# Kernel optimization log

Measured on AMD Instinct MI355X. Metric: run time of the kernel, lower is better.

The kernel has to match this reference:

```python
import jax, jax.numpy as jnp
import numpy as np

B, H, N, D, RPE = 2, 8, 4096, 64, 64
LAYERS = 3


def _rms(x):
    # SimpleRMSNorm: x / sqrt(mean(x^2) + eps), no learned scale
    return x / jnp.sqrt(jnp.mean(x * x, axis=-1, keepdims=True) + 1e-8)


def setup_inputs() -> dict:
    key = jax.random.key(0)
    ks = jax.random.split(key, 7)
    s = 1.0 / np.sqrt(RPE)
    return {
        "x": jax.random.normal(ks[0], (B, H, N, D), dtype=jnp.float32),
        "w_in": jax.random.normal(ks[1], (1, RPE), dtype=jnp.float32) * 0.5,
        "b_in": jax.random.normal(ks[2], (RPE,), dtype=jnp.float32) * 0.02,
        "w_hid": jax.random.normal(ks[3], (LAYERS, RPE, RPE), dtype=jnp.float32) * s,
        "b_hid": jax.random.normal(ks[4], (LAYERS, RPE), dtype=jnp.float32) * 0.02,
        "w_out": jax.random.normal(ks[5], (RPE, H * D), dtype=jnp.float32) * s,
        "b_out": jax.random.normal(ks[6], (H * D,), dtype=jnp.float32) * 0.02,
    }


def reference(x, w_in, b_in, w_hid, b_hid, w_out, b_out):
    n = x.shape[-2]
    dt = x.dtype

    def rpe(idx):  # idx: (m, 1) relative-position features
        h = idx @ w_in + b_in  # (m, RPE)
        for i in range(LAYERS):  # non-residual: x = layer(x)
            h = jax.nn.relu(_rms(h)) @ w_hid[i] + b_hid[i]
        h = jax.nn.relu(_rms(h)) @ w_out + b_out  # (m, H*D)
        return h.reshape(-1, H, D).transpose(1, 0, 2)  # (H, m, D)

    zero_idx = jnp.ones((1, 1), dt)
    pos_idx = (1.0 / jnp.arange(2, n + 1, dtype=dt)).reshape(n - 1, 1)
    neg_idx = (-1.0 / jnp.arange(n, 1, -1, dtype=dt)).reshape(n - 1, 1)

    zero_k = rpe(zero_idx)  # (H, 1, D); used for both T[0] slots like the torch code
    a = jnp.concatenate([zero_k, rpe(pos_idx), zero_k, rpe(neg_idx)], axis=1)  # (H, 2n, D)
    # act_type='none' -> identity activation on a

    # Toeplitz matvec as circular conv of length 2n via FFT
    y = jnp.fft.rfft(x, 2 * n, axis=-2)          # (B, H, n+1, D) complex
    v = jnp.fft.rfft(a, 2 * n, axis=-2)[None]    # (1, H, n+1, D) complex
    out = jnp.fft.irfft(v * y, 2 * n, axis=-2)[:, :, :n, :]
    return out.astype(dt)
```

## Files before the change

### kernel.cpp

```cpp
#include <hip/hip_runtime.h>

#define N_SEQ 4096
#define N_FFT 8192
#define LAYERS 3
#define FT 512

#define IDX2(i) ((i) + (((i) >> 5) << 1))

#define WSYNC() { asm volatile("s_waitcnt lgkmcnt(0)" ::: "memory"); __builtin_amdgcn_wave_barrier(); }

__device__ __forceinline__ float2 cmulf(float2 a, float2 b) {
    return make_float2(fmaf(a.x, b.x, -a.y * b.y), fmaf(a.x, b.y, a.y * b.x));
}
__device__ __forceinline__ float2 cmulcf(float2 a, float2 b) {
    return make_float2(fmaf(a.x, b.x, a.y * b.y), fmaf(a.y, b.x, -a.x * b.y));
}
__device__ __forceinline__ float2 f2a(float2 a, float2 b) { return make_float2(a.x + b.x, a.y + b.y); }
__device__ __forceinline__ float2 f2s(float2 a, float2 b) { return make_float2(a.x - b.x, a.y - b.y); }

__device__ __forceinline__ void twchain(int np, float2* T)
{
    float c1, s1;
    __sincosf(-7.6699039394282061e-4f * (float)np, &s1, &c1);
    T[1] = make_float2(c1, s1);
    T[2] = cmulf(T[1], T[1]);
    T[3] = cmulf(T[2], T[1]);
    T[4] = cmulf(T[2], T[2]);
    T[5] = cmulf(T[3], T[2]);
    T[6] = cmulf(T[3], T[3]);
    T[7] = cmulf(T[4], T[3]);
}

__device__ __forceinline__ void ahead8(const float* x, int np, float2* X)
{
    const float R2 = 0.70710678118654752f;
    float p0 = x[0] + x[4], q0 = x[0] - x[4];
    float p1 = x[2] + x[6], q1 = x[2] - x[6];
    float r0 = x[1] + x[5], t0 = x[1] - x[5];
    float r1 = x[3] + x[7], t1 = x[3] - x[7];
    float e0 = p0 + p1, e2 = p0 - p1;
    float o0 = r0 + r1, o2 = r0 - r1;
    float rm = R2 * (t0 - t1), rp = R2 * (t0 + t1);
    X[0] = make_float2(e0 + o0, 0.f);
    X[4] = make_float2(e0 - o0, 0.f);
    X[2] = make_float2(e2, -o2);
    X[6] = make_float2(e2,  o2);
    X[1] = make_float2(q0 + rm, -q1 - rp);
    X[5] = make_float2(q0 - rm, -q1 + rp);
    X[3] = make_float2(q0 - rm,  q1 - rp);
    X[7] = make_float2(q0 + rm,  q1 + rp);
    float2 T[8];
    twchain(np, T);
#pragma unroll
    for (int q = 1; q < 8; ++q) X[q] = cmulf(X[q], T[q]);
}

__device__ __forceinline__ void zhead8(const float2* z, int np, float2* X)
{
    const float R2 = 0.70710678118654752f;
    float2 A0 = f2a(z[0], z[2]);
    float2 A2 = f2s(z[0], z[2]);
    float2 A1 = make_float2(z[0].x + z[2].y, z[0].y - z[2].x);
    float2 A3 = make_float2(z[0].x - z[2].y, z[0].y + z[2].x);
    float2 B0 = f2a(z[1], z[3]);
    float2 bm = f2s(z[1], z[3]);
    float2 B2 = make_float2(bm.y, -bm.x);
    float2 u1 = make_float2(z[1].x + z[3].y, z[1].y - z[3].x);
    float2 B1 = make_float2(R2 * (u1.x + u1.y), R2 * (u1.y - u1.x));
    float2 u3 = make_float2(z[1].x - z[3].y, z[1].y + z[3].x);
    float2 B3 = make_float2(R2 * (u3.y - u3.x), -R2 * (u3.x + u3.y));
    X[0] = f2a(A0, B0); X[4] = f2s(A0, B0);
    X[1] = f2a(A1, B1); X[5] = f2s(A1, B1);
    X[2] = f2a(A2, B2); X[6] = f2s(A2, B2);
    X[3] = f2a(A3, B3); X[7] = f2s(A3, B3);
    float2 T[8];
    twchain(np, T);
#pragma unroll
    for (int q = 1; q < 8; ++q) X[q] = cmulf(X[q], T[q]);
}

__device__ __forceinline__ void ihead8(const float2* v, int np, float2* u)
{
    const float R2 = 0.70710678118654752f;
    float2 T[8];
    twchain(np, T);
    float2 V[8];
    V[0] = v[0];
#pragma unroll
    for (int q = 1; q < 8; ++q) V[q] = cmulcf(v[q], T[q]);
    float2 s0 = f2a(V[0], V[4]), d0 = f2s(V[0], V[4]);
    float2 s1 = f2a(V[1], V[5]), d1 = f2s(V[1], V[5]);
    float2 s2 = f2a(V[2], V[6]), d2 = f2s(V[2], V[6]);
    float2 s3 = f2a(V[3], V[7]), d3 = f2s(V[3], V[7]);
    u[0] = f2a(f2a(s0, s1), f2a(s2, s3));
    u[2] = make_float2((s0.x - s2.x) - (s1.y - s3.y),
                       (s0.y - s2.y) + (s1.x - s3.x));
    float m1 = R2 * (d1.x - d1.y), p1 = R2 * (d1.x + d1.y);
    float m3 = R2 * (d3.x - d3.y), p3 = R2 * (d3.x + d3.y);
    u[1] = make_float2(d0.x + m1 - d2.y - p3, d0.y + p1 + d2.x + m3);
    u[3] = make_float2(d0.x - p1 + d2.y + m3, d0.y + m1 - d2.x + p3);
}

__device__ __forceinline__ void tail4_fwd(float2* y)
{
#pragma unroll
    for (int g = 0; g < 16; g += 4) {
        float2 a = f2a(y[g],     y[g + 2]);
        float2 b = f2s(y[g],     y[g + 2]);
        float2 c = f2a(y[g + 1], y[g + 3]);
        float2 w = f2s(y[g + 1], y[g + 3]);
        float2 d = make_float2(w.y, -w.x);
        y[g]     = f2a(a, c);
        y[g + 1] = f2a(b, d);
        y[g + 2] = f2s(a, c);
        y[g + 3] = f2s(b, d);
    }
}
__device__ __forceinline__ void tail4_inv(float2* y)
{
#pragma unroll
    for (int g = 0; g < 16; g += 4) {
        float2 a = f2a(y[g],     y[g + 2]);
        float2 b = f2s(y[g],     y[g + 2]);
        float2 c = f2a(y[g + 1], y[g + 3]);
        float2 d = f2s(y[g + 1], y[g + 3]);
        float2 id = make_float2(-d.y, d.x);
        y[g]     = f2a(a, c);
        y[g + 2] = f2s(a, c);
        y[g + 1] = f2a(b, id);
        y[g + 3] = f2s(b, id);
    }
}

template<int M>
__device__ __forceinline__ void wpass16_fwd(float2* buf, int C, int lane)
{
    const int Q = M >> 4;
    const int j = lane & (Q - 1);
    const int base = C + (lane / Q) * M + j;
    const float KR[4] = {1.f, 0.9238795325f, 0.7071067812f, 0.3826834324f};
    const float KI[4] = {0.f, -0.3826834324f, -0.7071067812f, -0.9238795325f};
    float xr[4][4], xi[4][4];
#pragma unroll
    for (int a = 0; a < 4; ++a)
#pragma unroll
        for (int b = 0; b < 4; ++b) {
            float2 v = buf[IDX2(base + a * (M >> 2) + b * Q)];
            xr[a][b] = v.x; xi[a][b] = v.y;
        }
    float cj, sj;
    __sincosf(-6.283185307179586f / (float)M * (float)j, &sj, &cj);
#pragma unroll
    for (int b = 0; b < 4; ++b) {
        float c1 = cj * KR[b] - sj * KI[b];
        float s1 = cj * KI[b] + sj * KR[b];
        float c2 = c1 * c1 - s1 * s1, s2 = 2.f * c1 * s1;
        float c3 = c2 * c1 - s2 * s1, s3 = c2 * s1 + s2 * c1;
        float ar = xr[0][b] + xr[2][b], ai = xi[0][b] + xi[2][b];
        float br = xr[0][b] - xr[2][b], bi = xi[0][b] - xi[2][b];
        float cr = xr[1][b] + xr[3][b], ci = xi[1][b] + xi[3][b];
        float dr = xi[1][b] - xi[3][b], di = -(xr[1][b] - xr[3][b]);
        xr[0][b] = ar + cr;               xi[0][b] = ai + ci;
        float t1r = br + dr, t1i = bi + di;
        xr[1][b] = t1r * c1 - t1i * s1;   xi[1][b] = t1r * s1 + t1i * c1;
        float t2r = ar - cr, t2i = ai - ci;
        xr[2][b] = t2r * c2 - t2i * s2;   xi[2][b] = t2r * s2 + t2i * c2;
        float t3r = br - dr, t3i = bi - di;
        xr[3][b] = t3r * c3 - t3i * s3;   xi[3][b] = t3r * s3 + t3i * c3;
    }
    {
        float e1c = cj * cj - sj * sj, e1s = 2.f * cj * sj;
        float c1 = e1c * e1c - e1s * e1s, s1 = 2.f * e1c * e1s;
        float c2 = c1 * c1 - s1 * s1, s2 = 2.f * c1 * s1;
        float c3 = c2 * c1 - s2 * s1, s3 = c2 * s1 + s2 * c1;
#pragma unroll
        for (int a = 0; a < 4; ++a) {
            float ar = xr[a][0] + xr[a][2], ai = xi[a][0] + xi[a][2];
            float br = xr[a][0] - xr[a][2], bi = xi[a][0] - xi[a][2];
            float cr = xr[a][1] + xr[a][3], ci = xi[a][1] + xi[a][3];
            float dr = xi[a][1] - xi[a][3], di = -(xr[a][1] - xr[a][3]);
            xr[a][0] = ar + cr;               xi[a][0] = ai + ci;
            float t1r = br + dr, t1i = bi + di;
            xr[a][1] = t1r * c1 - t1i * s1;   xi[a][1] = t1r * s1 + t1i * c1;
            float t2r = ar - cr, t2i = ai - ci;
            xr[a][2] = t2r * c2 - t2i * s2;   xi[a][2] = t2r * s2 + t2i * c2;
            float t3r = br - dr, t3i = bi - di;
            xr[a][3] = t3r * c3 - t3i * s3;   xi[a][3] = t3r * s3 + t3i * c3;
        }
    }
#pragma unroll
    for (int a = 0; a < 4; ++a)
#pragma unroll
        for (int b = 0; b < 4; ++b)
            buf[IDX2(base + a * (M >> 2) + b * Q)] = make_float2(xr[a][b], xi[a][b]);
}

template<int M>
__device__ __forceinline__ void wpass16_inv(float2* buf, int C, int lane)
{
    const int Q = M >> 4;
    const int j = lane & (Q - 1);
    const int base = C + (lane / Q) * M + j;
    const float KR[4] = {1.f, 0.9238795325f, 0.7071067812f, 0.3826834324f};
    const float KI[4] = {0.f, 0.3826834324f, 0.7071067812f, 0.9238795325f};
    float xr[4][4], xi[4][4];
#pragma unroll
    for (int a = 0; a < 4; ++a)
#pragma unroll
        for (int b = 0; b < 4; ++b) {
            float2 v = buf[IDX2(base + a * (M >> 2) + b * Q)];
            xr[a][b] = v.x; xi[a][b] = v.y;
        }
    float cj, sj;
    __sincosf(6.283185307179586f / (float)M * (float)j, &sj, &cj);
    {
        float e1c = cj * cj - sj * sj, e1s = 2.f * cj * sj;
        float c1 = e1c * e1c - e1s * e1s, s1 = 2.f * e1c * e1s;
        float c2 = c1 * c1 - s1 * s1, s2 = 2.f * c1 * s1;
        float c3 = c2 * c1 - s2 * s1, s3 = c2 * s1 + s2 * c1;
#pragma unroll
        for (int a = 0; a < 4; ++a) {
            float t0r = xr[a][0], t0i = xi[a][0];
            float t1r = xr[a][1] * c1 - xi[a][1] * s1, t1i = xr[a][1] * s1 + xi[a][1] * c1;
            float t2r = xr[a][2] * c2 - xi[a][2] * s2, t2i = xr[a][2] * s2 + xi[a][2] * c2;
            float t3r = xr[a][3] * c3 - xi[a][3] * s3, t3i = xr[a][3] * s3 + xi[a][3] * c3;
            float pr = t0r + t2r, pi = t0i + t2i;
            float qr = t0r - t2r, qi = t0i - t2i;
            float rr = t1r + t3r, ri = t1i + t3i;
            float sr = -(t1i - t3i), si = t1r - t3r;
            xr[a][0] = pr + rr; xi[a][0] = pi + ri;
            xr[a][1] = qr + sr; xi[a][1] = qi + si;
            xr[a][2] = pr - rr; xi[a][2] = pi - ri;
            xr[a][3] = qr - sr; xi[a][3] = qi - si;
        }
    }
#pragma unroll
    for (int b = 0; b < 4; ++b) {
        float c1 = cj * KR[b] - sj * KI[b];
        float s1 = cj * KI[b] + sj * KR[b];
        float c2 = c1 * c1 - s1 * s1, s2 = 2.f * c1 * s1;
        float c3 = c2 * c1 - s2 * s1, s3 = c2 * s1 + s2 * c1;
        float t0r = xr[0][b], t0i = xi[0][b];
        float t1r = xr[1][b] * c1 - xi[1][b] * s1, t1i = xr[1][b] * s1 + xi[1][b] * c1;
        float t2r = xr[2][b] * c2 - xi[2][b] * s2, t2i = xr[2][b] * s2 + xi[2][b] * c2;
        float t3r = xr[3][b] * c3 - xi[3][b] * s3, t3i = xr[3][b] * s3 + xi[3][b] * c3;
        float pr = t0r + t2r, pi = t0i + t2i;
        float qr = t0r - t2r, qi = t0i - t2i;
        float rr = t1r + t3r, ri = t1i + t3i;
        float sr = -(t1i - t3i), si = t1r - t3r;
        xr[0][b] = pr + rr; xi[0][b] = pi + ri;
        xr[1][b] = qr + sr; xi[1][b] = qi + si;
        xr[2][b] = pr - rr; xi[2][b] = pi - ri;
        xr[3][b] = qr - sr; xi[3][b] = qi - si;
    }
#pragma unroll
    for (int a = 0; a < 4; ++a)
#pragma unroll
        for (int b = 0; b < 4; ++b)
            buf[IDX2(base + a * (M >> 2) + b * Q)] = make_float2(xr[a][b], xi[a][b]);
}

__global__ __launch_bounds__(512, 2) void prep_kernel(
    const float* __restrict__ x,
    const float* __restrict__ w_in, const float* __restrict__ b_in,
    const float* __restrict__ w_hid, const float* __restrict__ b_hid,
    const float* __restrict__ w_out, const float* __restrict__ b_out,
    float* __restrict__ a_t, float2* __restrict__ xt2)
{
    __shared__ __align__(16) char smem[43264];
    const int tid = threadIdx.x;

    if (blockIdx.x >= 256) {
        float (*t0)[65] = (float (*)[65])smem;
        float (*t1)[65] = (float (*)[65])(smem + 16640);
        int bb = blockIdx.x - 256;
        int h = bb >> 6;
        int nb = bb & 63;
        int lx = tid & 63;
        int ly = tid >> 6;
        const float* s0 = x + ((size_t)h * N_SEQ + nb * 64) * 64;
        const float* s1 = x + ((size_t)(8 + h) * N_SEQ + nb * 64) * 64;
        for (int r = ly; r < 64; r += 8) {
            t0[r][lx] = s0[r * 64 + lx];
            t1[r][lx] = s1[r * 64 + lx];
        }
        __syncthreads();
        for (int r = ly; r < 64; r += 8) {
            float2* dst = xt2 + (size_t)(h * 64 + r) * N_SEQ + nb * 64;
            dst[lx] = make_float2(t0[lx][r], t1[lx][r]);
        }
        return;
    }

    float (*ubuf)[65] = (float (*)[65])smem;
    float (*sums)[17] = (float (*)[17])(smem + 8320);
    float4* wl        = (float4*)(smem + 10496);

    {
        const int p = tid & 31;
        const int s = tid >> 5;
        const int pos = blockIdx.x * 32 + p;
        float v;
        if (pos == 0 || pos == N_SEQ) v = 1.0f;
        else if (pos < N_SEQ)         v = 1.0f / (float)(pos + 1);
        else                          v = -1.0f / (float)(2 * N_SEQ + 1 - pos);

        float h[4];
#pragma unroll
        for (int i = 0; i < 4; ++i) {
            int f = s * 4 + i;
            h[i] = v * w_in[f] + b_in[f];
        }
        for (int L = 0; L < LAYERS; ++L) {
            const float4* wsrc = (const float4*)(w_hid + L * 4096);
            wl[tid] = wsrc[tid];
            wl[tid + 512] = wsrc[tid + 512];
            float s2 = h[0]*h[0] + h[1]*h[1] + h[2]*h[2] + h[3]*h[3];
            sums[p][s] = s2;
            __syncthreads();
            float tot = 0.f;
#pragma unroll
            for (int g = 0; g < 16; ++g) tot += sums[p][g];
            float r = rsqrtf(tot * (1.f / 64.f) + 1e-8f);
#pragma unroll
            for (int i = 0; i < 4; ++i)
                ubuf[p][s * 4 + i] = fmaxf(h[i] * r, 0.f);
            __syncthreads();
            float acc[4];
#pragma unroll
            for (int i = 0; i < 4; ++i) acc[i] = b_hid[L * 64 + s * 4 + i];
#pragma unroll 8
            for (int j = 0; j < 64; ++j) {
                float uj = ubuf[p][j];
                float4 w = wl[j * 16 + s];
                acc[0] = fmaf(uj, w.x, acc[0]); acc[1] = fmaf(uj, w.y, acc[1]);
                acc[2] = fmaf(uj, w.z, acc[2]); acc[3] = fmaf(uj, w.w, acc[3]);
            }
#pragma unroll
            for (int i = 0; i < 4; ++i) h[i] = acc[i];
            __syncthreads();
        }
        float s2 = h[0]*h[0] + h[1]*h[1] + h[2]*h[2] + h[3]*h[3];
        sums[p][s] = s2;
        __syncthreads();
        float tot = 0.f;
#pragma unroll
        for (int g = 0; g < 16; ++g) tot += sums[p][g];
        float r = rsqrtf(tot * (1.f / 64.f) + 1e-8f);
#pragma unroll
        for (int i = 0; i < 4; ++i)
            ubuf[p][s * 4 + i] = fmaxf(h[i] * r, 0.f);
        __syncthreads();
    }

    {
        const int o  = tid >> 3;
        const int pg = tid & 7;
        const int pos0 = blockIdx.x * 32;
        float4* wt = wl;
        float acc[8][4];
#pragma unroll
        for (int ii = 0; ii < 8; ++ii) {
            float bo = b_out[o * 8 + ii];
#pragma unroll
            for (int i = 0; i < 4; ++i) acc[ii][i] = bo;
        }
        for (int jc = 0; jc < 4; ++jc) {
            float4 wreg[4];
#pragma unroll
            for (int k = 0; k < 4; ++k) {
                int i4 = k * 512 + tid;
                int jj = i4 >> 7, f4 = i4 & 127;
                wreg[k] = *(const float4*)(w_out + (jc * 16 + jj) * 512 + f4 * 4);
            }
            __syncthreads();
#pragma unroll
            for (int k = 0; k < 4; ++k) {
                int i4 = k * 512 + tid;
                wt[i4] = wreg[k];
            }
            __syncthreads();
#pragma unroll
            for (int jj = 0; jj < 16; ++jj) {
                int j = jc * 16 + jj;
                float4 w0 = wt[jj * 128 + o * 2];
                float4 w1 = wt[jj * 128 + o * 2 + 1];
                float u0 = ubuf[pg * 4 + 0][j];
                float u1 = ubuf[pg * 4 + 1][j];
                float u2 = ubuf[pg * 4 + 2][j];
                float u3 = ubuf[pg * 4 + 3][j];
                acc[0][0] = fmaf(u0, w0.x, acc[0][0]); acc[0][1] = fmaf(u1, w0.x, acc[0][1]);
                acc[0][2] = fmaf(u2, w0.x, acc[0][2]); acc[0][3] = fmaf(u3, w0.x, acc[0][3]);
                acc[1][0] = fmaf(u0, w0.y, acc[1][0]); acc[1][1] = fmaf(u1, w0.y, acc[1][1]);
                acc[1][2] = fmaf(u2, w0.y, acc[1][2]); acc[1][3] = fmaf(u3, w0.y, acc[1][3]);
                acc[2][0] = fmaf(u0, w0.z, acc[2][0]); acc[2][1] = fmaf(u1, w0.z, acc[2][1]);
                acc[2][2] = fmaf(u2, w0.z, acc[2][2]); acc[2][3] = fmaf(u3, w0.z, acc[2][3]);
                acc[3][0] = fmaf(u0, w0.w, acc[3][0]); acc[3][1] = fmaf(u1, w0.w, acc[3][1]);
                acc[3][2] = fmaf(u2, w0.w, acc[3][2]); acc[3][3] = fmaf(u3, w0.w, acc[3][3]);
                acc[4][0] = fmaf(u0, w1.x, acc[4][0]); acc[4][1] = fmaf(u1, w1.x, acc[4][1]);
                acc[4][2] = fmaf(u2, w1.x, acc[4][2]); acc[4][3] = fmaf(u3, w1.x, acc[4][3]);
                acc[5][0] = fmaf(u0, w1.y, acc[5][0]); acc[5][1] = fmaf(u1, w1.y, acc[5][1]);
                acc[5][2] = fmaf(u2, w1.y, acc[5][2]); acc[5][3] = fmaf(u3, w1.y, acc[5][3]);
                acc[6][0] = fmaf(u0, w1.z, acc[6][0]); acc[6][1] = fmaf(u1, w1.z, acc[6][1]);
                acc[6][2] = fmaf(u2, w1.z, acc[6][2]); acc[6][3] = fmaf(u3, w1.z, acc[6][3]);
                acc[7][0] = fmaf(u0, w1.w, acc[7][0]); acc[7][1] = fmaf(u1, w1.w, acc[7][1]);
                acc[7][2] = fmaf(u2, w1.w, acc[7][2]); acc[7][3] = fmaf(u3, w1.w, acc[7][3]);
            }
            __syncthreads();
        }
#pragma unroll
        for (int ii = 0; ii < 8; ++ii) {
            int f = o * 8 + ii;
#pragma unroll
            for (int i = 0; i < 4; ++i)
                a_t[(size_t)f * N_FFT + pos0 + pg * 4 + i] = acc[ii][i];
        }
    }
}

__global__ __launch_bounds__(FT, 2) void conv_kernel(const float* __restrict__ a_t,
                                                     const float2* __restrict__ xt2,
                                                     float2* __restrict__ out_t2)
{
    __shared__ __align__(16) float2 buf[8704];
    const int tid = threadIdx.x;
    const int lane = tid & 63;
    const int C = (tid >> 6) << 10;
    const int hd = blockIdx.x;

    {
        const float2* asrc = (const float2*)(a_t + (size_t)hd * N_FFT);
        float2 av[8];
#pragma unroll
        for (int p = 0; p < 8; ++p) av[p] = asrc[tid + 512 * p];
        float xa[8], xb[8];
#pragma unroll
        for (int p = 0; p < 8; ++p) { xa[p] = av[p].x; xb[p] = av[p].y; }
        float2 X0[8], X1[8];
        ahead8(xa, 2 * tid,     X0);
        ahead8(xb, 2 * tid + 1, X1);
#pragma unroll
        for (int q = 0; q < 8; ++q)
            *(float4*)&buf[IDX2(q * 1024 + 2 * tid)] =
                make_float4(X0[q].x, X0[q].y, X1[q].x, X1[q].y);
    }
    __syncthreads();
    wpass16_fwd<1024>(buf, C, lane);
    WSYNC();
    wpass16_fwd<64>(buf, C, lane);
    WSYNC();
    float2 asp[16];
#pragma unroll
    for (int k = 0; k < 8; ++k) {
        float4 v = *(const float4*)&buf[IDX2(C + 16 * lane + 2 * k)];
        asp[2 * k]     = make_float2(v.x, v.y);
        asp[2 * k + 1] = make_float2(v.z, v.w);
    }
    tail4_fwd(asp);
    float4 zl[4];
    {
        const float4* zsrc = (const float4*)(xt2 + (size_t)hd * N_SEQ);
#pragma unroll
        for (int p = 0; p < 4; ++p) zl[p] = zsrc[tid + 512 * p];
    }
    __syncthreads();
    {
        float2 z0[4], z1[4];
#pragma unroll
        for (int p = 0; p < 4; ++p) {
            z0[p] = make_float2(zl[p].x, zl[p].y);
            z1[p] = make_float2(zl[p].z, zl[p].w);
        }
        float2 X0[8], X1[8];
        zhead8(z0, 2 * tid,     X0);
        zhead8(z1, 2 * tid + 1, X1);
#pragma unroll
        for (int q = 0; q < 8; ++q)
            *(float4*)&buf[IDX2(q * 1024 + 2 * tid)] =
                make_float4(X0[q].x, X0[q].y, X1[q].x, X1[q].y);
    }
    __syncthreads();
    wpass16_fwd<1024>(buf, C, lane);
    WSYNC();
    wpass16_fwd<64>(buf, C, lane);
    WSYNC();
    {
        float2 zp[16];
#pragma unroll
        for (int k = 0; k < 8; ++k) {
            float4 v = *(const float4*)&buf[IDX2(C + 16 * lane + 2 * k)];
            zp[2 * k]     = make_float2(v.x, v.y);
            zp[2 * k + 1] = make_float2(v.z, v.w);
        }
        tail4_fwd(zp);
        const float inv = 1.0f / (float)N_FFT;
#pragma unroll
        for (int c = 0; c < 16; ++c) {
            float2 m = cmulf(zp[c], asp[c]);
            zp[c] = make_float2(m.x * inv, m.y * inv);
        }
        tail4_inv(zp);
#pragma unroll
        for (int k = 0; k < 8; ++k)
            *(float4*)&buf[IDX2(C + 16 * lane + 2 * k)] =
                make_float4(zp[2 * k].x, zp[2 * k].y, zp[2 * k + 1].x, zp[2 * k + 1].y);
    }
    WSYNC();
    wpass16_inv<64>(buf, C, lane);
    WSYNC();
    wpass16_inv<1024>(buf, C, lane);
    __syncthreads();
    {
        float2 v0[8], v1[8];
#pragma unroll
        for (int q = 0; q < 8; ++q) {
            float4 r = *(const float4*)&buf[IDX2(q * 1024 + 2 * tid)];
            v0[q] = make_float2(r.x, r.y);
            v1[q] = make_float2(r.z, r.w);
        }
        float2 u0[4], u1[4];
        ihead8(v0, 2 * tid,     u0);
        ihead8(v1, 2 * tid + 1, u1);
        float4* dst = (float4*)(out_t2 + (size_t)hd * N_SEQ);
#pragma unroll
        for (int p = 0; p < 4; ++p)
            dst[tid + 512 * p] = make_float4(u0[p].x, u0[p].y, u1[p].x, u1[p].y);
    }
}

__global__ __launch_bounds__(256) void transpose_o_kernel(const float2* __restrict__ out_t2,
                                                          float* __restrict__ out)
{
    __shared__ float t0[64][65];
    __shared__ float t1[64][65];
    int h = blockIdx.x >> 6;
    int nb = blockIdx.x & 63;
    int lx = threadIdx.x & 63;
    int ly = threadIdx.x >> 6;
    for (int r = ly; r < 64; r += 4) {
        float2 v = out_t2[(size_t)(h * 64 + r) * N_SEQ + nb * 64 + lx];
        t0[r][lx] = v.x;
        t1[r][lx] = v.y;
    }
    __syncthreads();
    float* d0 = out + ((size_t)h * N_SEQ + nb * 64) * 64;
    float* d1 = out + ((size_t)(8 + h) * N_SEQ + nb * 64) * 64;
    for (int r = ly; r < 64; r += 4) {
        d0[r * 64 + lx] = t0[lx][r];
        d1[r * 64 + lx] = t1[lx][r];
    }
}

extern "C" void kernel_launch(void* const* d_in, const int* in_sizes, int n_in,
                              void* d_out, int out_size, void* d_ws, size_t ws_size,
                              hipStream_t stream)
{
    const float* x     = (const float*)d_in[0];
    const float* w_in  = (const float*)d_in[1];
    const float* b_in  = (const float*)d_in[2];
    const float* w_hid = (const float*)d_in[3];
    const float* b_hid = (const float*)d_in[4];
    const float* w_out = (const float*)d_in[5];
    const float* b_out = (const float*)d_in[6];
    float* out = (float*)d_out;

    char* ws = (char*)d_ws;
    float2* xt2    = (float2*)ws;
    float*  a_t    = (float*)(ws + (size_t)16 * 1024 * 1024);
    float2* out_t2 = (float2*)(ws + (size_t)32 * 1024 * 1024);

    prep_kernel<<<768, 512, 0, stream>>>(x, w_in, b_in, w_hid, b_hid, w_out, b_out,
                                         a_t, xt2);
    conv_kernel<<<512, FT, 0, stream>>>(a_t, xt2, out_t2);
    transpose_o_kernel<<<512, 256, 0, stream>>>(out_t2, out);
}
```

Baseline: 149.3 us.

## Split kernel FFT of the RPE filter into a separate kernel

Splits the fused conv kernel into two launches. The first computes the frequency spectrum of each filter column and writes it to a new workspace buffer. The second loads that spectrum from global memory while it transforms x, multiplies, and runs the inverse FFT. The aim is to shorten the conv kernel and lower its register pressure by no longer keeping the filter spectrum live across the x FFT. In exchange it adds a kernel launch and 32 MB of extra global write and read traffic.

```diff
diff --git a/kernel.cpp b/kernel.cpp
--- a/kernel.cpp
+++ b/kernel.cpp
@@ -8,6 +8,7 @@
 #define IDX2(i) ((i) + (((i) >> 5) << 1))
 
 #define WSYNC() { asm volatile("s_waitcnt lgkmcnt(0)" ::: "memory"); __builtin_amdgcn_wave_barrier(); }
+
 
 __device__ __forceinline__ float2 cmulf(float2 a, float2 b) {
     return make_float2(fmaf(a.x, b.x, -a.y * b.y), fmaf(a.x, b.y, a.y * b.x));
@@ -418,9 +419,8 @@
     }
 }
 
-__global__ __launch_bounds__(FT, 2) void conv_kernel(const float* __restrict__ a_t,
-                                                     const float2* __restrict__ xt2,
-                                                     float2* __restrict__ out_t2)
+__global__ __launch_bounds__(FT, 2) void afft_kernel(const float* __restrict__ a_t,
+                                                     float2* __restrict__ aspec)
 {
     __shared__ __align__(16) float2 buf[8704];
     const int tid = threadIdx.x;
@@ -449,22 +449,38 @@
     WSYNC();
     wpass16_fwd<64>(buf, C, lane);
     WSYNC();
-    float2 asp[16];
-#pragma unroll
-    for (int k = 0; k < 8; ++k) {
-        float4 v = *(const float4*)&buf[IDX2(C + 16 * lane + 2 * k)];
-        asp[2 * k]     = make_float2(v.x, v.y);
-        asp[2 * k + 1] = make_float2(v.z, v.w);
-    }
-    tail4_fwd(asp);
-    float4 zl[4];
+    {
+        float2 asp[16];
+#pragma unroll
+        for (int k = 0; k < 8; ++k) {
+            float4 v = *(const float4*)&buf[IDX2(C + 16 * lane + 2 * k)];
+            asp[2 * k]     = make_float2(v.x, v.y);
+            asp[2 * k + 1] = make_float2(v.z, v.w);
+        }
+        tail4_fwd(asp);
+        float4* dst = (float4*)(aspec + (size_t)hd * N_FFT) + tid * 8;
+#pragma unroll
+        for (int k = 0; k < 8; ++k)
+            dst[k] = make_float4(asp[2 * k].x, asp[2 * k].y,
+                                 asp[2 * k + 1].x, asp[2 * k + 1].y);
+    }
+}
+
+__global__ __launch_bounds__(FT, 2) void zconv_kernel(const float2* __restrict__ aspec,
+                                                      const float2* __restrict__ xt2,
+                                                      float2* __restrict__ out_t2)
+{
+    __shared__ __align__(16) float2 buf[8704];
+    const int tid = threadIdx.x;
+    const int lane = tid & 63;
+    const int C = (tid >> 6) << 10;
+    const int hd = blockIdx.x;
+
     {
         const float4* zsrc = (const float4*)(xt2 + (size_t)hd * N_SEQ);
+        float4 zl[4];
 #pragma unroll
         for (int p = 0; p < 4; ++p) zl[p] = zsrc[tid + 512 * p];
-    }
-    __syncthreads();
-    {
         float2 z0[4], z1[4];
 #pragma unroll
         for (int p = 0; p < 4; ++p) {
@@ -485,6 +501,10 @@
     wpass16_fwd<64>(buf, C, lane);
     WSYNC();
     {
+        const float4* ap = (const float4*)(aspec + (size_t)hd * N_FFT) + tid * 8;
+        float4 aw[8];
+#pragma unroll
+        for (int k = 0; k < 8; ++k) aw[k] = ap[k];
         float2 zp[16];
 #pragma unroll
         for (int k = 0; k < 8; ++k) {
@@ -495,9 +515,13 @@
         tail4_fwd(zp);
         const float inv = 1.0f / (float)N_FFT;
 #pragma unroll
-        for (int c = 0; c < 16; ++c) {
-            float2 m = cmulf(zp[c], asp[c]);
-            zp[c] = make_float2(m.x * inv, m.y * inv);
+        for (int k = 0; k < 8; ++k) {
+            float2 a0 = make_float2(aw[k].x, aw[k].y);
+            float2 a1 = make_float2(aw[k].z, aw[k].w);
+            float2 m0 = cmulf(zp[2 * k],     a0);
+            float2 m1 = cmulf(zp[2 * k + 1], a1);
+            zp[2 * k]     = make_float2(m0.x * inv, m0.y * inv);
+            zp[2 * k + 1] = make_float2(m1.x * inv, m1.y * inv);
         }
         tail4_inv(zp);
 #pragma unroll
@@ -568,9 +592,11 @@
     float2* xt2    = (float2*)ws;
     float*  a_t    = (float*)(ws + (size_t)16 * 1024 * 1024);
     float2* out_t2 = (float2*)(ws + (size_t)32 * 1024 * 1024);
+    float2* aspec  = (float2*)(ws + (size_t)48 * 1024 * 1024);
 
     prep_kernel<<<768, 512, 0, stream>>>(x, w_in, b_in, w_hid, b_hid, w_out, b_out,
                                          a_t, xt2);
-    conv_kernel<<<512, FT, 0, stream>>>(a_t, xt2, out_t2);
+    afft_kernel<<<512, FT, 0, stream>>>(a_t, aspec);
+    zconv_kernel<<<512, FT, 0, stream>>>(aspec, xt2, out_t2);
     transpose_o_kernel<<<512, 256, 0, stream>>>(out_t2, out);
 }
```

Measured after the change: 151.4 us. No clear change (+1.4%).
